# Kernel tuning notes

Hardware: AMD Instinct MI355X
Metric: run time of the kernel (lower is better)

Reference implementation:

```python
import jax, jax.numpy as jnp
import numpy as np

OUT_FEATURES = 12288
IN_FEATURES = 4096
GROUP_SIZE = 4096


def _dequant_weight(weight_q4, weight_norm):
    # weight_q4: [G, group_size//2] packed bytes (two 4-bit nibbles each)
    # weight_norm: [G, 1] fp16 per-group max-abs
    low = jnp.bitwise_and(weight_q4, 15)          # even positions
    high = jnp.bitwise_and(weight_q4 >> 4, 15)    # odd positions
    # interleave: [..., k, 2] -> [..., 2k]
    q16 = jnp.stack([low, high], axis=-1).reshape(weight_q4.shape[0], -1)
    norm = weight_norm.astype(jnp.float16)
    w = (q16.astype(jnp.float16) / jnp.float16(15)) * (jnp.float16(2) * norm) - norm
    return w.reshape(OUT_FEATURES, IN_FEATURES)


def setup_inputs() -> dict:
    key = jax.random.key(0)
    k1, k2, k3, k4 = jax.random.split(key, 4)
    G = OUT_FEATURES * IN_FEATURES // GROUP_SIZE
    x = (jax.random.normal(k1, (8, 2048, IN_FEATURES), dtype=jnp.float32) * 0.1).astype(jnp.float16)
    weight_q4 = jax.random.randint(k2, (G, GROUP_SIZE // 2), 0, 256, dtype=jnp.int32)
    weight_norm = (jax.random.uniform(k3, (G, 1), dtype=jnp.float32) * 0.05 + 0.01).astype(jnp.float16)
    bias = (jax.random.normal(k4, (OUT_FEATURES,), dtype=jnp.float32) * 0.02).astype(jnp.float16)
    return {"x": x, "weight_q4": weight_q4, "weight_norm": weight_norm, "bias": bias}


def reference(x, weight_q4, weight_norm, bias):
    w = _dequant_weight(weight_q4, weight_norm)  # [out, in] fp16
    # F.linear(x, w, bias) == x @ w.T + bias
    y = jnp.einsum("bsi,oi->bso", x, w, preferred_element_type=jnp.float32).astype(jnp.float16)
    return y + bias
```

## Files before the change

### kernel.cpp

```cpp
#include <hip/hip_runtime.h>
#include <hip/hip_bf16.h>
#include <stdint.h>

#define M_TOT 16384
#define N_TOT 12288
#define K_TOT 4096

typedef __bf16 bf16;
typedef __bf16 bf16x8 __attribute__((ext_vector_type(8)));
typedef float f32x4 __attribute__((ext_vector_type(4)));

typedef __attribute__((address_space(1))) const void gvoid;
typedef __attribute__((address_space(3))) void lvoid;

__device__ __forceinline__ void async_copy16(const void* g, void* l) {
    __builtin_amdgcn_global_load_lds((gvoid*)g, (lvoid*)l, 16, 0, 0);
}

__global__ __launch_bounds__(256) void convert_x_kernel(
        const float* __restrict__ x, bf16* __restrict__ xb) {
    size_t t = (size_t)blockIdx.x * 256 + threadIdx.x;
    const float4* xv = (const float4*)x;
    float4 a = xv[2 * t], b = xv[2 * t + 1];
    bf16x8 o = { (bf16)a.x, (bf16)a.y, (bf16)a.z, (bf16)a.w,
                 (bf16)b.x, (bf16)b.y, (bf16)b.z, (bf16)b.w };
    ((bf16x8*)xb)[t] = o;
}

__global__ __launch_bounds__(256) void dequant_kernel(
        const int* __restrict__ wq, const float* __restrict__ norm,
        bf16* __restrict__ wout) {
    int t = blockIdx.x * 256 + threadIdx.x;
    int4 qw = ((const int4*)wq)[t];
    int row = t >> 9;
    float n = norm[row];
    float s = n * (2.0f / 15.0f);
    int v[4] = {qw.x, qw.y, qw.z, qw.w};
    bf16x8 o;
#pragma unroll
    for (int u = 0; u < 4; ++u) {
        o[2*u]   = (bf16)((float)(v[u] & 15)        * s - n);
        o[2*u+1] = (bf16)((float)((v[u] >> 4) & 15) * s - n);
    }
    ((bf16x8*)wout)[t] = o;
}

template <bool FUSED>
__global__ __launch_bounds__(256, 2) void gemm_kernel(
        const bf16*  __restrict__ Ab,
        const float* __restrict__ Af,
        const bf16*  __restrict__ Wb,
        const int*   __restrict__ Wq,
        const float* __restrict__ norm,
        const float* __restrict__ bias,
        float*       __restrict__ C)
{
    __shared__ bf16 As[8 * 128 * 8];
    __shared__ bf16 Bs[8 * 128 * 8];
    __shared__ float Bnorm[128];

    const int tid  = threadIdx.x;
    const int m0   = blockIdx.y * 128;
    const int n0   = blockIdx.x * 128;
    const int lane = tid & 63;
    const int wave = tid >> 6;
    const int wm = wave & 1, wn = wave >> 1;
    const int lm = lane & 15, q = lane >> 4;

    if (FUSED) {
        if (tid < 128) Bnorm[tid] = norm[n0 + tid];
        __syncthreads();
    }

    f32x4 acc[4][4];
#pragma unroll
    for (int i = 0; i < 4; ++i)
#pragma unroll
        for (int j = 0; j < 4; ++j) acc[i][j] = (f32x4){0.f, 0.f, 0.f, 0.f};

    for (int k0 = 0; k0 < K_TOT; k0 += 64) {
#pragma unroll
        for (int it = 0; it < 4; ++it) {
            int ci = it * 256 + tid;
            int cb = ci >> 7, row = ci & 127;
            if (!FUSED) {
                async_copy16(Ab + (size_t)(m0 + row) * K_TOT + k0 + cb * 8,
                             &As[ci * 8]);
            } else {
                const float4* p = (const float4*)(Af + (size_t)(m0 + row) * K_TOT
                                                  + k0 + cb * 8);
                float4 a = p[0], b = p[1];
                bf16x8 o = { (bf16)a.x, (bf16)a.y, (bf16)a.z, (bf16)a.w,
                             (bf16)b.x, (bf16)b.y, (bf16)b.z, (bf16)b.w };
                *(bf16x8*)&As[ci * 8] = o;
            }
        }
#pragma unroll
        for (int it = 0; it < 4; ++it) {
            int ci = it * 256 + tid;
            int cb = ci >> 7, row = ci & 127;
            if (!FUSED) {
                async_copy16(Wb + (size_t)(n0 + row) * K_TOT + k0 + cb * 8,
                             &Bs[ci * 8]);
            } else {
                int4 qw = *(const int4*)(Wq + (size_t)(n0 + row) * (K_TOT / 2)
                                         + (k0 >> 1) + cb * 4);
                float n = Bnorm[row];
                float s = n * (2.0f / 15.0f);
                int v[4] = {qw.x, qw.y, qw.z, qw.w};
                bf16x8 o;
#pragma unroll
                for (int u = 0; u < 4; ++u) {
                    o[2*u]   = (bf16)((float)(v[u] & 15)        * s - n);
                    o[2*u+1] = (bf16)((float)((v[u] >> 4) & 15) * s - n);
                }
                *(bf16x8*)&Bs[ci * 8] = o;
            }
        }
        __syncthreads();

#pragma unroll
        for (int ks = 0; ks < 2; ++ks) {
            bf16x8 af[4], bfr[4];
            int cb = ks * 4 + q;
#pragma unroll
            for (int i = 0; i < 4; ++i) {
                int row = wm * 64 + i * 16 + lm;
                af[i] = *(const bf16x8*)&As[(cb * 128 + row) * 8];
            }
#pragma unroll
            for (int j = 0; j < 4; ++j) {
                int row = wn * 64 + j * 16 + lm;
                bfr[j] = *(const bf16x8*)&Bs[(cb * 128 + row) * 8];
            }
#pragma unroll
            for (int i = 0; i < 4; ++i)
#pragma unroll
                for (int j = 0; j < 4; ++j)
                    acc[i][j] = __builtin_amdgcn_mfma_f32_16x16x32_bf16(
                        af[i], bfr[j], acc[i][j], 0, 0, 0);
        }
        __syncthreads();
    }

    float bj[4];
#pragma unroll
    for (int j = 0; j < 4; ++j)
        bj[j] = bias[n0 + wn * 64 + j * 16 + lm];
#pragma unroll
    for (int i = 0; i < 4; ++i) {
#pragma unroll
        for (int r = 0; r < 4; ++r) {
            size_t row  = (size_t)(m0 + wm * 64 + i * 16 + q * 4 + r);
            size_t base = row * N_TOT + n0 + wn * 64 + lm;
#pragma unroll
            for (int j = 0; j < 4; ++j)
                C[base + j * 16] = acc[i][j][r] + bj[j];
        }
    }
}

extern "C" void kernel_launch(void* const* d_in, const int* in_sizes, int n_in,
                              void* d_out, int out_size, void* d_ws, size_t ws_size,
                              hipStream_t stream) {
    const float* x    = (const float*)d_in[0];
    const int*   wq   = (const int*)d_in[1];
    const float* norm = (const float*)d_in[2];
    const float* bias = (const float*)d_in[3];
    float* out = (float*)d_out;

    const size_t WBYTES = (size_t)N_TOT * K_TOT * sizeof(bf16);
    const size_t XBYTES = (size_t)M_TOT * K_TOT * sizeof(bf16);
    dim3 grid(N_TOT / 128, M_TOT / 128);

    if (ws_size >= WBYTES + XBYTES) {
        bf16* wdq = (bf16*)d_ws;
        bf16* xb  = (bf16*)((char*)d_ws + WBYTES);
        dequant_kernel<<<(N_TOT * (K_TOT / 2) / 4) / 256, 256, 0, stream>>>(
            wq, norm, wdq);
        convert_x_kernel<<<(M_TOT * K_TOT / 8) / 256, 256, 0, stream>>>(x, xb);
        gemm_kernel<false><<<grid, 256, 0, stream>>>(xb, nullptr, wdq, nullptr,
                                                     nullptr, bias, out);
    } else {
        gemm_kernel<true><<<grid, 256, 0, stream>>>(nullptr, x, nullptr, wq,
                                                    norm, bias, out);
    }
}
```

Before: 3.882 ms.

## Enlarge GEMM tiles to 256x256 with double-buffered LDS and XCD-aware block mapping

Grows the GEMM block tile from 128x128 to 256x256 with 512 threads, so each wave computes a 128x64 sub-tile and arithmetic intensity per loaded byte rises. Shared-memory staging is double-buffered so the next K-slice is prefetched while MFMAs run on the current one. A 1D grid is remapped so consecutive blocks on each XCD share M rows, which is meant to improve L2 reuse. Output stores become nontemporal. The costs are higher register pressure (32 accumulator fragments plus 8 A fragments) and 128KB of LDS per block, which may limit occupancy or cause spills.

```diff
diff --git a/kernel.cpp b/kernel.cpp
--- a/kernel.cpp
+++ b/kernel.cpp
@@ -5,6 +5,9 @@
 #define M_TOT 16384
 #define N_TOT 12288
 #define K_TOT 4096
+#define BM 256
+#define BN 256
+#define BK 64
 
 typedef __bf16 bf16;
 typedef __bf16 bf16x8 __attribute__((ext_vector_type(8)));
@@ -46,7 +49,7 @@
 }
 
 template <bool FUSED>
-__global__ __launch_bounds__(256, 2) void gemm_kernel(
+__global__ __launch_bounds__(512, 2) void gemm_kernel(
         const bf16*  __restrict__ Ab,
         const float* __restrict__ Af,
         const bf16*  __restrict__ Wb,
@@ -55,92 +58,104 @@
         const float* __restrict__ bias,
         float*       __restrict__ C)
 {
-    __shared__ bf16 As[8 * 128 * 8];
-    __shared__ bf16 Bs[8 * 128 * 8];
-    __shared__ float Bnorm[128];
-
-    const int tid  = threadIdx.x;
-    const int m0   = blockIdx.y * 128;
-    const int n0   = blockIdx.x * 128;
+    __shared__ bf16 As[2][(BK / 8) * BM * 8];
+    __shared__ bf16 Bs[2][(BK / 8) * BN * 8];
+
+    const int tid = threadIdx.x;
+
+    const int lin = blockIdx.x;
+    const int xcd = lin & 7;
+    const int s   = lin >> 3;
+    const int bn  = s % 48;
+    const int bm  = xcd * 8 + s / 48;
+    const int m0  = bm * BM;
+    const int n0  = bn * BN;
+
     const int lane = tid & 63;
     const int wave = tid >> 6;
-    const int wm = wave & 1, wn = wave >> 1;
+    const int wm = wave >> 2, wn = wave & 3;
     const int lm = lane & 15, q = lane >> 4;
 
-    if (FUSED) {
-        if (tid < 128) Bnorm[tid] = norm[n0 + tid];
-        __syncthreads();
-    }
-
-    f32x4 acc[4][4];
-#pragma unroll
-    for (int i = 0; i < 4; ++i)
+    f32x4 acc[8][4];
+#pragma unroll
+    for (int i = 0; i < 8; ++i)
 #pragma unroll
         for (int j = 0; j < 4; ++j) acc[i][j] = (f32x4){0.f, 0.f, 0.f, 0.f};
 
-    for (int k0 = 0; k0 < K_TOT; k0 += 64) {
+    auto stage = [&](int b, int k0) {
 #pragma unroll
         for (int it = 0; it < 4; ++it) {
-            int ci = it * 256 + tid;
-            int cb = ci >> 7, row = ci & 127;
+            int ci = it * 512 + tid;
+            int cb = ci >> 8, row = ci & 255;
             if (!FUSED) {
                 async_copy16(Ab + (size_t)(m0 + row) * K_TOT + k0 + cb * 8,
-                             &As[ci * 8]);
+                             &As[b][ci * 8]);
             } else {
                 const float4* p = (const float4*)(Af + (size_t)(m0 + row) * K_TOT
                                                   + k0 + cb * 8);
-                float4 a = p[0], b = p[1];
+                float4 a = p[0], c = p[1];
                 bf16x8 o = { (bf16)a.x, (bf16)a.y, (bf16)a.z, (bf16)a.w,
-                             (bf16)b.x, (bf16)b.y, (bf16)b.z, (bf16)b.w };
-                *(bf16x8*)&As[ci * 8] = o;
+                             (bf16)c.x, (bf16)c.y, (bf16)c.z, (bf16)c.w };
+                *(bf16x8*)&As[b][ci * 8] = o;
             }
         }
 #pragma unroll
         for (int it = 0; it < 4; ++it) {
-            int ci = it * 256 + tid;
-            int cb = ci >> 7, row = ci & 127;
+            int ci = it * 512 + tid;
+            int cb = ci >> 8, row = ci & 255;
             if (!FUSED) {
                 async_copy16(Wb + (size_t)(n0 + row) * K_TOT + k0 + cb * 8,
-                             &Bs[ci * 8]);
+                             &Bs[b][ci * 8]);
             } else {
                 int4 qw = *(const int4*)(Wq + (size_t)(n0 + row) * (K_TOT / 2)
                                          + (k0 >> 1) + cb * 4);
-                float n = Bnorm[row];
-                float s = n * (2.0f / 15.0f);
+                float n = norm[n0 + row];
+                float sc = n * (2.0f / 15.0f);
                 int v[4] = {qw.x, qw.y, qw.z, qw.w};
                 bf16x8 o;
 #pragma unroll
                 for (int u = 0; u < 4; ++u) {
-                    o[2*u]   = (bf16)((float)(v[u] & 15)        * s - n);
-                    o[2*u+1] = (bf16)((float)((v[u] >> 4) & 15) * s - n);
+                    o[2*u]   = (bf16)((float)(v[u] & 15)        * sc - n);
+                    o[2*u+1] = (bf16)((float)((v[u] >> 4) & 15) * sc - n);
                 }
-                *(bf16x8*)&Bs[ci * 8] = o;
-            }
-        }
-        __syncthreads();
+                *(bf16x8*)&Bs[b][ci * 8] = o;
+            }
+        }
+    };
+
+    stage(0, 0);
+    asm volatile("s_waitcnt vmcnt(0)" ::: "memory");
+    __syncthreads();
+
+    int cur = 0;
+    for (int k0 = 0; k0 < K_TOT; k0 += BK) {
+        if (k0 + BK < K_TOT) stage(cur ^ 1, k0 + BK);
 
 #pragma unroll
         for (int ks = 0; ks < 2; ++ks) {
-            bf16x8 af[4], bfr[4];
+            bf16x8 af[8], bfr[4];
             int cb = ks * 4 + q;
 #pragma unroll
-            for (int i = 0; i < 4; ++i) {
-                int row = wm * 64 + i * 16 + lm;
-                af[i] = *(const bf16x8*)&As[(cb * 128 + row) * 8];
+            for (int i = 0; i < 8; ++i) {
+                int row = wm * 128 + i * 16 + lm;
+                af[i] = *(const bf16x8*)&As[cur][(cb * BM + row) * 8];
             }
 #pragma unroll
             for (int j = 0; j < 4; ++j) {
                 int row = wn * 64 + j * 16 + lm;
-                bfr[j] = *(const bf16x8*)&Bs[(cb * 128 + row) * 8];
-            }
-#pragma unroll
-            for (int i = 0; i < 4; ++i)
+                bfr[j] = *(const bf16x8*)&Bs[cur][(cb * BN + row) * 8];
+            }
+#pragma unroll
+            for (int i = 0; i < 8; ++i)
 #pragma unroll
                 for (int j = 0; j < 4; ++j)
                     acc[i][j] = __builtin_amdgcn_mfma_f32_16x16x32_bf16(
                         af[i], bfr[j], acc[i][j], 0, 0, 0);
         }
+
+        asm volatile("s_waitcnt vmcnt(0)" ::: "memory");
         __syncthreads();
+        cur ^= 1;
     }
 
     float bj[4];
@@ -148,14 +163,15 @@
     for (int j = 0; j < 4; ++j)
         bj[j] = bias[n0 + wn * 64 + j * 16 + lm];
 #pragma unroll
-    for (int i = 0; i < 4; ++i) {
+    for (int i = 0; i < 8; ++i) {
 #pragma unroll
         for (int r = 0; r < 4; ++r) {
-            size_t row  = (size_t)(m0 + wm * 64 + i * 16 + q * 4 + r);
+            size_t row  = (size_t)(m0 + wm * 128 + i * 16 + q * 4 + r);
             size_t base = row * N_TOT + n0 + wn * 64 + lm;
 #pragma unroll
             for (int j = 0; j < 4; ++j)
-                C[base + j * 16] = acc[i][j][r] + bj[j];
+                __builtin_nontemporal_store(acc[i][j][r] + bj[j],
+                                            &C[base + j * 16]);
         }
     }
 }
@@ -171,7 +187,7 @@
 
     const size_t WBYTES = (size_t)N_TOT * K_TOT * sizeof(bf16);
     const size_t XBYTES = (size_t)M_TOT * K_TOT * sizeof(bf16);
-    dim3 grid(N_TOT / 128, M_TOT / 128);
+    const int nblocks = (M_TOT / BM) * (N_TOT / BN);
 
     if (ws_size >= WBYTES + XBYTES) {
         bf16* wdq = (bf16*)d_ws;
@@ -179,10 +195,10 @@
         dequant_kernel<<<(N_TOT * (K_TOT / 2) / 4) / 256, 256, 0, stream>>>(
             wq, norm, wdq);
         convert_x_kernel<<<(M_TOT * K_TOT / 8) / 256, 256, 0, stream>>>(x, xb);
-        gemm_kernel<false><<<grid, 256, 0, stream>>>(xb, nullptr, wdq, nullptr,
-                                                     nullptr, bias, out);
+        gemm_kernel<false><<<nblocks, 512, 0, stream>>>(xb, nullptr, wdq, nullptr,
+                                                        nullptr, bias, out);
     } else {
-        gemm_kernel<true><<<grid, 256, 0, stream>>>(nullptr, x, nullptr, wq,
-                                                    norm, bias, out);
-    }
-}
+        gemm_kernel<true><<<nblocks, 512, 0, stream>>>(nullptr, x, nullptr, wq,
+                                                       norm, bias, out);
+    }
+}
```

Result: faster. 3.638 ms (-6.3%).
